# Kernel optimization log

Measured on AMD Instinct MI355X. Metric: run time of the kernel, lower is better.

## Reference

```python
import jax, jax.numpy as jnp
import numpy as np

NUM_EMBEDDINGS = 1024
EMBEDDING_DIM = 64
COMMITMENT_COST = 0.25


def setup_inputs() -> dict:
    key = jax.random.key(0)
    k1, k2 = jax.random.split(key)
    inputs = jax.random.normal(k1, (32, 4096, EMBEDDING_DIM), dtype=jnp.float32)
    embeddings = jax.random.normal(k2, (NUM_EMBEDDINGS, EMBEDDING_DIM), dtype=jnp.float32)
    return {"inputs": inputs, "embeddings": embeddings}


def _l2_normalize(x, axis=-1, eps=1e-12):
    # matches F.normalize(p=2): x / max(||x||, eps)
    n = jnp.sqrt(jnp.sum(x * x, axis=axis, keepdims=True))
    return x / jnp.maximum(n, eps)


def reference(inputs, embeddings):
    input_shape = inputs.shape
    flat = inputs.reshape(-1, EMBEDDING_DIM)            # [N, D]
    flat_n = _l2_normalize(flat, axis=1)                # [N, D]
    emb_n = _l2_normalize(embeddings, axis=1)           # [K, D]

    # squared euclidean distances between normalized vectors: [N, K]
    d = (jnp.sum(flat_n * flat_n, axis=1, keepdims=True)
         + jnp.sum(emb_n * emb_n, axis=1)
         - 2.0 * flat_n @ emb_n.T)
    idx = jnp.argmin(d, axis=1)                         # [N] int

    quantized = embeddings[idx]                         # [N, D] gather

    e_latent_loss = jnp.mean((jax.lax.stop_gradient(quantized) - flat) ** 2)
    # straight-through estimator
    quantized_ste = flat + jax.lax.stop_gradient(quantized - flat)
    q_latent_loss = jnp.mean((quantized_ste - jax.lax.stop_gradient(flat)) ** 2)
    vq_loss = q_latent_loss + COMMITMENT_COST * e_latent_loss

    quantized_out = quantized_ste.reshape(input_shape)

    counts = jnp.bincount(idx, length=NUM_EMBEDDINGS).astype(jnp.float32)
    avg_probs = counts / idx.shape[0]
    perplexity = jnp.exp(-jnp.sum(avg_probs * jnp.log(avg_probs + 1e-10)))
    codebook_usage = jnp.sum(avg_probs > 0).astype(jnp.float32) / NUM_EMBEDDINGS

    return quantized_out, idx, vq_loss, perplexity, codebook_usage
```

## Files before the change

kernel.cpp:

```cpp
#include <hip/hip_runtime.h>
#include <hip/hip_bf16.h>

#define NQ       131072
#define KC       1024
#define DIM      64
#define MARGIN_A 7.5e-5f
#define RGRID    2048

typedef __attribute__((ext_vector_type(8))) short  s8bf;
typedef __attribute__((ext_vector_type(4))) float  f32x4;

union BF8 { s8bf v; unsigned short u[8]; };

__device__ __forceinline__ unsigned short f2bf_u(float f) {
    union { __hip_bfloat16 h; unsigned short u; } cv;
    cv.h = __float2bfloat16(f);
    return cv.u;
}
__device__ __forceinline__ float bfu2f(unsigned short u) {
    union { __hip_bfloat16 h; unsigned short u; } cv;
    cv.u = u;
    return __bfloat162float(cv.h);
}

__global__ __launch_bounds__(256) void k_prep(const float* __restrict__ emb,
                                              unsigned short* __restrict__ wB,
                                              double* __restrict__ eT,
                                              double* __restrict__ wB2D,
                                              int* __restrict__ counts,
                                              int* __restrict__ nflag,
                                              float* __restrict__ lossp) {
    const int tid = threadIdx.x;
    if (blockIdx.x == 0) {
        #pragma unroll
        for (int i = 0; i < 4; ++i) counts[tid * 4 + i] = 0;
        if (tid == 0) { *nflag = 0; *lossp = 0.f; }
    }
    int c = blockIdx.x * 256 + tid;
    if (c >= KC) return;
    float e[DIM];
    const float4* ep = reinterpret_cast<const float4*>(emb + (size_t)c * DIM);
    #pragma unroll
    for (int i = 0; i < 16; ++i) {
        float4 t = ep[i];
        e[4*i+0] = t.x; e[4*i+1] = t.y; e[4*i+2] = t.z; e[4*i+3] = t.w;
    }
    float s = 0.f;
    #pragma unroll
    for (int i = 0; i < DIM; ++i) s += e[i] * e[i];
    float inv = 1.0f / fmaxf(sqrtf(s), 1e-12f);
    const int t = c >> 4, col = c & 15;
    #pragma unroll
    for (int k = 0; k < DIM; ++k) {
        float h = e[k] * inv;
        unsigned short hi = f2bf_u(h);
        unsigned short lo = f2bf_u(h - bfu2f(hi));
        int s_ = k >> 5, g = (k >> 3) & 3, j = k & 7;
        int ln = col + 16 * g;
        wB[((t*4 + s_*2 + 0) * 64 + ln) * 8 + j] = hi;
        wB[((t*4 + s_*2 + 1) * 64 + ln) * 8 + j] = lo;
    }
    double sd = 0.0;
    #pragma unroll
    for (int i = 0; i < DIM; ++i) sd += (double)e[i] * (double)e[i];
    double dnd = fmax(sqrt(sd), 1e-12);
    double b2 = 0.0;
    #pragma unroll
    for (int i = 0; i < DIM; ++i) {
        double eh = (double)e[i] / dnd;
        eT[(size_t)i * KC + c] = eh;
        b2 += eh * eh;
    }
    wB2D[c] = b2;
}

__global__ __launch_bounds__(256) void k_assign(const float* __restrict__ inp,
                                                const unsigned short* __restrict__ wB,
                                                float* __restrict__ idx_out,
                                                int* __restrict__ flag_list,
                                                int* __restrict__ nflag) {
    const int tid  = threadIdx.x;
    const int lane = tid & 63, wv = tid >> 6;
    const int col  = lane & 15, g  = lane >> 4;
    const int qbase = blockIdx.x * 128 + wv * 32;

    BF8 ah[2][2], al[2][2];
    #pragma unroll
    for (int s = 0; s < 2; ++s) {
        const float4* q4 = reinterpret_cast<const float4*>(inp + (size_t)(qbase + 16*s + col) * DIM);
        float4 xa = q4[2*g], xb = q4[2*g + 1], ya = q4[8 + 2*g], yb = q4[9 + 2*g];
        float x[16] = { xa.x, xa.y, xa.z, xa.w, xb.x, xb.y, xb.z, xb.w,
                        ya.x, ya.y, ya.z, ya.w, yb.x, yb.y, yb.z, yb.w };
        float sq = 0.f;
        #pragma unroll
        for (int i = 0; i < 16; ++i) sq += x[i] * x[i];
        sq += __shfl_xor(sq, 16);
        sq += __shfl_xor(sq, 32);
        float ninv = -1.0f / fmaxf(sqrtf(sq), 1e-12f);
        #pragma unroll
        for (int i = 0; i < 8; ++i) {
            float h0 = x[i] * ninv, h1 = x[8 + i] * ninv;
            unsigned short hi0 = f2bf_u(h0);
            unsigned short hi1 = f2bf_u(h1);
            ah[s][0].u[i] = hi0;  al[s][0].u[i] = f2bf_u(h0 - bfu2f(hi0));
            ah[s][1].u[i] = hi1;  al[s][1].u[i] = f2bf_u(h1 - bfu2f(hi1));
        }
    }

    int best[2][4], best2[2][4];
    #pragma unroll
    for (int s = 0; s < 2; ++s)
        #pragma unroll
        for (int r = 0; r < 4; ++r) { best[s][r] = 0x7FFFFFFF; best2[s][r] = 0x7FFFFFFF; }

    const s8bf* wBs = reinterpret_cast<const s8bf*>(wB);
    s8bf nb0 = wBs[0*64 + lane];
    s8bf nb1 = wBs[1*64 + lane];
    s8bf nb2 = wBs[2*64 + lane];
    s8bf nb3 = wBs[3*64 + lane];

    for (int gt = 0; gt < 64; ++gt) {
        s8bf bh0 = nb0, bl0 = nb1, bh1 = nb2, bl1 = nb3;
        if (gt < 63) {
            const s8bf* p = wBs + (gt + 1) * 4 * 64 + lane;
            nb0 = p[0]; nb1 = p[64]; nb2 = p[128]; nb3 = p[192];
        }
        #pragma unroll
        for (int s = 0; s < 2; ++s) {
            f32x4 acc = {1.5f, 1.5f, 1.5f, 1.5f};
            acc = __builtin_amdgcn_mfma_f32_16x16x32_bf16(ah[s][0].v, bh0, acc, 0, 0, 0);
            acc = __builtin_amdgcn_mfma_f32_16x16x32_bf16(ah[s][1].v, bh1, acc, 0, 0, 0);
            acc = __builtin_amdgcn_mfma_f32_16x16x32_bf16(ah[s][0].v, bl0, acc, 0, 0, 0);
            acc = __builtin_amdgcn_mfma_f32_16x16x32_bf16(ah[s][1].v, bl1, acc, 0, 0, 0);
            acc = __builtin_amdgcn_mfma_f32_16x16x32_bf16(al[s][0].v, bh0, acc, 0, 0, 0);
            acc = __builtin_amdgcn_mfma_f32_16x16x32_bf16(al[s][1].v, bh1, acc, 0, 0, 0);
            #pragma unroll
            for (int r = 0; r < 4; ++r) {
                int p = (__float_as_int(acc[r]) & 0xFFFFFFC0) | gt;
                int bo = best[s][r];
                int b2n;
                asm("v_med3_i32 %0, %1, %2, %3"
                    : "=v"(b2n) : "v"(bo), "v"(best2[s][r]), "v"(p));
                best2[s][r] = b2n;
                best[s][r]  = min(bo, p);
            }
        }
    }

    int colb[2][4];
    #pragma unroll
    for (int s = 0; s < 2; ++s)
        #pragma unroll
        for (int r = 0; r < 4; ++r) colb[s][r] = col;

    #pragma unroll
    for (int s = 0; s < 2; ++s) {
        #pragma unroll
        for (int off = 1; off < 16; off <<= 1) {
            #pragma unroll
            for (int r = 0; r < 4; ++r) {
                int ob  = __shfl_xor(best[s][r],  off);
                int ob2 = __shfl_xor(best2[s][r], off);
                int oc  = __shfl_xor(colb[s][r],  off);
                int bo  = best[s][r];
                colb[s][r]  = (ob < bo) ? oc : colb[s][r];
                best[s][r]  = min(bo, ob);
                best2[s][r] = min(min(best2[s][r], ob2), max(bo, ob));
            }
        }
        #pragma unroll
        for (int r = 0; r < 4; ++r) {
            if (col == r) {
                int   q  = qbase + 16*s + 4*g + r;
                int   pk = best[s][r];
                float a1 = __int_as_float(pk & 0xFFFFFFC0);
                float a2 = __int_as_float(best2[s][r] & 0xFFFFFFC0);
                int code = ((pk & 63) << 4) | colb[s][r];
                idx_out[q] = (float)code;
                if (a2 - a1 < MARGIN_A) {
                    int slot = atomicAdd(nflag, 1);
                    flag_list[slot] = q;
                }
            }
        }
    }
}

__global__ __launch_bounds__(256) void k_rescue(const float* __restrict__ inp,
                                                const double* __restrict__ eT,
                                                const double* __restrict__ wB2D,
                                                const int* __restrict__ flag_list,
                                                const int* __restrict__ nflag,
                                                float* __restrict__ idx_out) {
    __shared__ double xh[DIM];
    __shared__ double Ash;
    __shared__ double sdw[4];
    __shared__ int    siw[4];
    const int tid = threadIdx.x;
    const int lane = tid & 63, wv = tid >> 6;
    const int n = *nflag;

    for (int j = blockIdx.x; j < n; j += gridDim.x) {
        const int q = flag_list[j];
        if (tid < 64) {
            double xv = (double)inp[(size_t)q * DIM + tid];
            double s = xv * xv;
            #pragma unroll
            for (int off = 32; off; off >>= 1) s += __shfl_xor(s, off);
            double dn = fmax(sqrt(s), 1e-12);
            double h  = xv / dn;
            xh[tid] = h;
            double a = h * h;
            #pragma unroll
            for (int off = 32; off; off >>= 1) a += __shfl_xor(a, off);
            if (tid == 0) Ash = a;
        }
        __syncthreads();
        const double A = Ash;

        double dot0 = 0.0, dot1 = 0.0, dot2 = 0.0, dot3 = 0.0;
        #pragma unroll 8
        for (int i = 0; i < DIM; ++i) {
            double xi = xh[i];
            const double* row = eT + (size_t)i * KC + tid;
            dot0 += xi * row[0];
            dot1 += xi * row[256];
            dot2 += xi * row[512];
            dot3 += xi * row[768];
        }
        double bd = 1e300; int bi = 1 << 30;
        double d0 = (A + wB2D[tid      ]) - 2.0 * dot0;
        double d1 = (A + wB2D[tid + 256]) - 2.0 * dot1;
        double d2 = (A + wB2D[tid + 512]) - 2.0 * dot2;
        double d3 = (A + wB2D[tid + 768]) - 2.0 * dot3;
        if (d0 < bd) { bd = d0; bi = tid;       }
        if (d1 < bd) { bd = d1; bi = tid + 256; }
        if (d2 < bd) { bd = d2; bi = tid + 512; }
        if (d3 < bd) { bd = d3; bi = tid + 768; }
        #pragma unroll
        for (int off = 1; off < 64; off <<= 1) {
            double od = __shfl_xor(bd, off);
            int    oi = __shfl_xor(bi, off);
            if (od < bd || (od == bd && oi < bi)) { bd = od; bi = oi; }
        }
        if (lane == 0) { sdw[wv] = bd; siw[wv] = bi; }
        __syncthreads();
        if (tid == 0) {
            double B = sdw[0]; int I = siw[0];
            #pragma unroll
            for (int i = 1; i < 4; ++i)
                if (sdw[i] < B || (sdw[i] == B && siw[i] < I)) { B = sdw[i]; I = siw[i]; }
            idx_out[q] = (float)I;
        }
        __syncthreads();
    }
}

__global__ __launch_bounds__(256) void k_gather_loss(const float* __restrict__ inp,
                                                     const float* __restrict__ emb,
                                                     const float* __restrict__ idx_out,
                                                     float* __restrict__ qout,
                                                     float* __restrict__ loss,
                                                     int* __restrict__ counts) {
    __shared__ int h[KC];
    const int tid = threadIdx.x;
    for (int i = tid; i < KC; i += 256) h[i] = 0;
    __syncthreads();

    const int gid = blockIdx.x * 256 + tid;
    float lsum = 0.f;
    for (int e4 = gid; e4 < NQ * 16; e4 += 524288) {
        int   qi = e4 >> 4;
        int   d4 = e4 & 15;
        int   k  = ((int)idx_out[qi]) & (KC - 1);
        float4 qv = reinterpret_cast<const float4*>(emb + (size_t)k * DIM)[d4];
        float4 fv = reinterpret_cast<const float4*>(inp)[e4];
        float ux = qv.x - fv.x, uy = qv.y - fv.y, uz = qv.z - fv.z, uw = qv.w - fv.w;
        lsum += ux*ux + uy*uy + uz*uz + uw*uw;
        reinterpret_cast<float4*>(qout)[e4] = qv;
        if (d4 == 0) atomicAdd(&h[k], 1);
    }
    __syncthreads();
    for (int i = tid; i < KC; i += 256) {
        int v = h[i];
        if (v) atomicAdd(&counts[i], v);
    }
    #pragma unroll
    for (int off = 32; off; off >>= 1) lsum += __shfl_xor(lsum, off);
    __shared__ float wsum[4];
    int wid = tid >> 6, lane = tid & 63;
    if (lane == 0) wsum[wid] = lsum;
    __syncthreads();
    if (tid == 0)
        atomicAdd(loss, (wsum[0] + wsum[1]) + (wsum[2] + wsum[3]));
}

__global__ __launch_bounds__(1024) void k_stats2(const int* __restrict__ counts,
                                                 float* __restrict__ out3) {
    int t = threadIdx.x;
    int c = counts[t];
    float p    = (float)c * (1.0f / (float)NQ);
    float ent  = p * logf(p + 1e-10f);
    float used = (c > 0) ? 1.0f : 0.0f;
    #pragma unroll
    for (int off = 32; off; off >>= 1) {
        ent  += __shfl_xor(ent, off);
        used += __shfl_xor(used, off);
    }
    __shared__ float se[16], su[16];
    int w = t >> 6, l = t & 63;
    if (l == 0) { se[w] = ent; su[w] = used; }
    __syncthreads();
    if (t == 0) {
        float E = 0.f, U = 0.f;
        #pragma unroll
        for (int i = 0; i < 16; ++i) { E += se[i]; U += su[i]; }
        float L = out3[0];
        out3[0] = L * 1.25f / 8388608.0f;
        out3[1] = expf(-E);
        out3[2] = U * (1.0f / 1024.0f);
    }
}

extern "C" void kernel_launch(void* const* d_in, const int* in_sizes, int n_in,
                              void* d_out, int out_size, void* d_ws, size_t ws_size,
                              hipStream_t stream) {
    const float* inp = (const float*)d_in[0];
    const float* emb = (const float*)d_in[1];

    float*  qout      = (float*)d_out;
    int*    flag_list = (int*)d_out;
    double* eT        = (double*)((float*)d_out + 1048576);
    float*  idx_out   = (float*)d_out + 8388608;
    float*  out3      = (float*)d_out + 8519680;

    int*            counts = (int*)d_ws;
    unsigned short* wB     = (unsigned short*)((char*)d_ws + 4096);
    double*         wB2D   = (double*)((char*)d_ws + 266240);
    int*            nflag  = (int*)((char*)d_ws + 274432);

    hipLaunchKernelGGL(k_prep,        dim3(4),     dim3(256),  0, stream,
                       emb, wB, eT, wB2D, counts, nflag, out3);
    hipLaunchKernelGGL(k_assign,      dim3(1024),  dim3(256),  0, stream,
                       inp, wB, idx_out, flag_list, nflag);
    hipLaunchKernelGGL(k_rescue,      dim3(RGRID), dim3(256),  0, stream,
                       inp, eT, wB2D, flag_list, nflag, idx_out);
    hipLaunchKernelGGL(k_gather_loss, dim3(2048),  dim3(256),  0, stream,
                       inp, emb, idx_out, qout, out3, counts);
    hipLaunchKernelGGL(k_stats2,      dim3(1),     dim3(1024), 0, stream, counts, out3);
}
```

Before: 118.8 us.

## Switch assignment to 32x32x16 MFMA tiles and parallelize codebook prep per element

The assignment kernel now uses 32x32x16 bf16 MFMA instructions with a 32-code tile per iteration (32 iterations instead of 64). The codebook pre-pack layout and the A-operand register layout change to match. This halves the per-tile argmin bookkeeping per code and raises MFMA efficiency. The prep kernel also moves from one thread per code with serial loops to one 64-lane wave per code using shuffle reductions, which removes the long serial prologue. The larger accumulator raises register pressure, and the final cross-lane reduction now takes 5 shuffle steps over 16 values.

```diff
diff --git a/kernel.cpp b/kernel.cpp
--- a/kernel.cpp
+++ b/kernel.cpp
@@ -7,8 +7,8 @@
 #define MARGIN_A 7.5e-5f
 #define RGRID    2048
 
-typedef __attribute__((ext_vector_type(8))) short  s8bf;
-typedef __attribute__((ext_vector_type(4))) float  f32x4;
+typedef __attribute__((ext_vector_type(8)))  short s8bf;
+typedef __attribute__((ext_vector_type(16))) float f32x16;
 
 union BF8 { s8bf v; unsigned short u[8]; };
 
@@ -23,55 +23,43 @@
     return __bfloat162float(cv.h);
 }
 
-__global__ __launch_bounds__(256) void k_prep(const float* __restrict__ emb,
-                                              unsigned short* __restrict__ wB,
-                                              double* __restrict__ eT,
-                                              double* __restrict__ wB2D,
-                                              int* __restrict__ counts,
-                                              int* __restrict__ nflag,
-                                              float* __restrict__ lossp) {
-    const int tid = threadIdx.x;
-    if (blockIdx.x == 0) {
-        #pragma unroll
-        for (int i = 0; i < 4; ++i) counts[tid * 4 + i] = 0;
-        if (tid == 0) { *nflag = 0; *lossp = 0.f; }
-    }
-    int c = blockIdx.x * 256 + tid;
-    if (c >= KC) return;
-    float e[DIM];
-    const float4* ep = reinterpret_cast<const float4*>(emb + (size_t)c * DIM);
-    #pragma unroll
-    for (int i = 0; i < 16; ++i) {
-        float4 t = ep[i];
-        e[4*i+0] = t.x; e[4*i+1] = t.y; e[4*i+2] = t.z; e[4*i+3] = t.w;
-    }
-    float s = 0.f;
-    #pragma unroll
-    for (int i = 0; i < DIM; ++i) s += e[i] * e[i];
-    float inv = 1.0f / fmaxf(sqrtf(s), 1e-12f);
-    const int t = c >> 4, col = c & 15;
-    #pragma unroll
-    for (int k = 0; k < DIM; ++k) {
-        float h = e[k] * inv;
-        unsigned short hi = f2bf_u(h);
-        unsigned short lo = f2bf_u(h - bfu2f(hi));
-        int s_ = k >> 5, g = (k >> 3) & 3, j = k & 7;
-        int ln = col + 16 * g;
-        wB[((t*4 + s_*2 + 0) * 64 + ln) * 8 + j] = hi;
-        wB[((t*4 + s_*2 + 1) * 64 + ln) * 8 + j] = lo;
-    }
-    double sd = 0.0;
-    #pragma unroll
-    for (int i = 0; i < DIM; ++i) sd += (double)e[i] * (double)e[i];
+__global__ __launch_bounds__(64) void k_prep(const float* __restrict__ emb,
+                                             unsigned short* __restrict__ wB,
+                                             double* __restrict__ eT,
+                                             double* __restrict__ wB2D,
+                                             int* __restrict__ counts,
+                                             int* __restrict__ nflag,
+                                             float* __restrict__ lossp) {
+    const int c = blockIdx.x;
+    const int i = threadIdx.x;
+    if (i == 0) counts[c] = 0;
+    if (c == 0 && i == 0) { *nflag = 0; *lossp = 0.f; }
+
+    float e = emb[(size_t)c * DIM + i];
+    float sq = e * e;
+    #pragma unroll
+    for (int off = 1; off < 64; off <<= 1) sq += __shfl_xor(sq, off);
+    float inv = 1.0f / fmaxf(sqrtf(sq), 1e-12f);
+    float h = e * inv;
+    unsigned short hi = f2bf_u(h);
+    unsigned short lo = f2bf_u(h - bfu2f(hi));
+    const int t = c >> 5, col = c & 31;
+    const int ks = i >> 4, hh = (i >> 3) & 1, j = i & 7;
+    const int ln = col + 32 * hh;
+    wB[(((t*8 + ks*2 + 0) * 64) + ln) * 8 + j] = hi;
+    wB[(((t*8 + ks*2 + 1) * 64) + ln) * 8 + j] = lo;
+
+    double ed = (double)e;
+    double sd = ed * ed;
+    #pragma unroll
+    for (int off = 1; off < 64; off <<= 1) sd += __shfl_xor(sd, off);
     double dnd = fmax(sqrt(sd), 1e-12);
-    double b2 = 0.0;
-    #pragma unroll
-    for (int i = 0; i < DIM; ++i) {
-        double eh = (double)e[i] / dnd;
-        eT[(size_t)i * KC + c] = eh;
-        b2 += eh * eh;
-    }
-    wB2D[c] = b2;
+    double eh  = ed / dnd;
+    eT[(size_t)i * KC + c] = eh;
+    double b2 = eh * eh;
+    #pragma unroll
+    for (int off = 1; off < 64; off <<= 1) b2 += __shfl_xor(b2, off);
+    if (i == 0) wB2D[c] = b2;
 }
 
 __global__ __launch_bounds__(256) void k_assign(const float* __restrict__ inp,
@@ -81,106 +69,110 @@
                                                 int* __restrict__ nflag) {
     const int tid  = threadIdx.x;
     const int lane = tid & 63, wv = tid >> 6;
-    const int col  = lane & 15, g  = lane >> 4;
+    const int m  = lane & 31;
+    const int hh = lane >> 5;
     const int qbase = blockIdx.x * 128 + wv * 32;
 
-    BF8 ah[2][2], al[2][2];
-    #pragma unroll
-    for (int s = 0; s < 2; ++s) {
-        const float4* q4 = reinterpret_cast<const float4*>(inp + (size_t)(qbase + 16*s + col) * DIM);
-        float4 xa = q4[2*g], xb = q4[2*g + 1], ya = q4[8 + 2*g], yb = q4[9 + 2*g];
-        float x[16] = { xa.x, xa.y, xa.z, xa.w, xb.x, xb.y, xb.z, xb.w,
-                        ya.x, ya.y, ya.z, ya.w, yb.x, yb.y, yb.z, yb.w };
+    BF8 ah[4], al[4];
+    {
+        const float4* qp = reinterpret_cast<const float4*>(inp + (size_t)(qbase + m) * DIM);
+        float x[32];
+        #pragma unroll
+        for (int ks = 0; ks < 4; ++ks) {
+            float4 a = qp[4*ks + 2*hh];
+            float4 b = qp[4*ks + 2*hh + 1];
+            x[8*ks+0]=a.x; x[8*ks+1]=a.y; x[8*ks+2]=a.z; x[8*ks+3]=a.w;
+            x[8*ks+4]=b.x; x[8*ks+5]=b.y; x[8*ks+6]=b.z; x[8*ks+7]=b.w;
+        }
         float sq = 0.f;
         #pragma unroll
-        for (int i = 0; i < 16; ++i) sq += x[i] * x[i];
-        sq += __shfl_xor(sq, 16);
+        for (int i = 0; i < 32; ++i) sq += x[i] * x[i];
         sq += __shfl_xor(sq, 32);
         float ninv = -1.0f / fmaxf(sqrtf(sq), 1e-12f);
         #pragma unroll
-        for (int i = 0; i < 8; ++i) {
-            float h0 = x[i] * ninv, h1 = x[8 + i] * ninv;
-            unsigned short hi0 = f2bf_u(h0);
-            unsigned short hi1 = f2bf_u(h1);
-            ah[s][0].u[i] = hi0;  al[s][0].u[i] = f2bf_u(h0 - bfu2f(hi0));
-            ah[s][1].u[i] = hi1;  al[s][1].u[i] = f2bf_u(h1 - bfu2f(hi1));
-        }
-    }
-
-    int best[2][4], best2[2][4];
-    #pragma unroll
-    for (int s = 0; s < 2; ++s)
-        #pragma unroll
-        for (int r = 0; r < 4; ++r) { best[s][r] = 0x7FFFFFFF; best2[s][r] = 0x7FFFFFFF; }
+        for (int ks = 0; ks < 4; ++ks)
+            #pragma unroll
+            for (int j = 0; j < 8; ++j) {
+                float h = x[8*ks+j] * ninv;
+                unsigned short hi = f2bf_u(h);
+                ah[ks].u[j] = hi;
+                al[ks].u[j] = f2bf_u(h - bfu2f(hi));
+            }
+    }
+
+    int best[16], best2[16];
+    #pragma unroll
+    for (int r = 0; r < 16; ++r) { best[r] = 0x7FFFFFFF; best2[r] = 0x7FFFFFFF; }
 
     const s8bf* wBs = reinterpret_cast<const s8bf*>(wB);
-    s8bf nb0 = wBs[0*64 + lane];
-    s8bf nb1 = wBs[1*64 + lane];
-    s8bf nb2 = wBs[2*64 + lane];
-    s8bf nb3 = wBs[3*64 + lane];
-
-    for (int gt = 0; gt < 64; ++gt) {
+    s8bf nb0 = wBs[0*64 + lane], nb1 = wBs[1*64 + lane];
+    s8bf nb2 = wBs[2*64 + lane], nb3 = wBs[3*64 + lane];
+    s8bf nb4 = wBs[4*64 + lane], nb5 = wBs[5*64 + lane];
+    s8bf nb6 = wBs[6*64 + lane], nb7 = wBs[7*64 + lane];
+
+    for (int gt = 0; gt < 32; ++gt) {
         s8bf bh0 = nb0, bl0 = nb1, bh1 = nb2, bl1 = nb3;
-        if (gt < 63) {
-            const s8bf* p = wBs + (gt + 1) * 4 * 64 + lane;
-            nb0 = p[0]; nb1 = p[64]; nb2 = p[128]; nb3 = p[192];
-        }
-        #pragma unroll
-        for (int s = 0; s < 2; ++s) {
-            f32x4 acc = {1.5f, 1.5f, 1.5f, 1.5f};
-            acc = __builtin_amdgcn_mfma_f32_16x16x32_bf16(ah[s][0].v, bh0, acc, 0, 0, 0);
-            acc = __builtin_amdgcn_mfma_f32_16x16x32_bf16(ah[s][1].v, bh1, acc, 0, 0, 0);
-            acc = __builtin_amdgcn_mfma_f32_16x16x32_bf16(ah[s][0].v, bl0, acc, 0, 0, 0);
-            acc = __builtin_amdgcn_mfma_f32_16x16x32_bf16(ah[s][1].v, bl1, acc, 0, 0, 0);
-            acc = __builtin_amdgcn_mfma_f32_16x16x32_bf16(al[s][0].v, bh0, acc, 0, 0, 0);
-            acc = __builtin_amdgcn_mfma_f32_16x16x32_bf16(al[s][1].v, bh1, acc, 0, 0, 0);
-            #pragma unroll
-            for (int r = 0; r < 4; ++r) {
-                int p = (__float_as_int(acc[r]) & 0xFFFFFFC0) | gt;
-                int bo = best[s][r];
-                int b2n;
-                asm("v_med3_i32 %0, %1, %2, %3"
-                    : "=v"(b2n) : "v"(bo), "v"(best2[s][r]), "v"(p));
-                best2[s][r] = b2n;
-                best[s][r]  = min(bo, p);
-            }
-        }
-    }
-
-    int colb[2][4];
-    #pragma unroll
-    for (int s = 0; s < 2; ++s)
-        #pragma unroll
-        for (int r = 0; r < 4; ++r) colb[s][r] = col;
-
-    #pragma unroll
-    for (int s = 0; s < 2; ++s) {
-        #pragma unroll
-        for (int off = 1; off < 16; off <<= 1) {
-            #pragma unroll
-            for (int r = 0; r < 4; ++r) {
-                int ob  = __shfl_xor(best[s][r],  off);
-                int ob2 = __shfl_xor(best2[s][r], off);
-                int oc  = __shfl_xor(colb[s][r],  off);
-                int bo  = best[s][r];
-                colb[s][r]  = (ob < bo) ? oc : colb[s][r];
-                best[s][r]  = min(bo, ob);
-                best2[s][r] = min(min(best2[s][r], ob2), max(bo, ob));
-            }
-        }
-        #pragma unroll
-        for (int r = 0; r < 4; ++r) {
-            if (col == r) {
-                int   q  = qbase + 16*s + 4*g + r;
-                int   pk = best[s][r];
-                float a1 = __int_as_float(pk & 0xFFFFFFC0);
-                float a2 = __int_as_float(best2[s][r] & 0xFFFFFFC0);
-                int code = ((pk & 63) << 4) | colb[s][r];
-                idx_out[q] = (float)code;
-                if (a2 - a1 < MARGIN_A) {
-                    int slot = atomicAdd(nflag, 1);
-                    flag_list[slot] = q;
-                }
+        s8bf bh2 = nb4, bl2 = nb5, bh3 = nb6, bl3 = nb7;
+        if (gt < 31) {
+            const s8bf* p = wBs + (size_t)(gt + 1) * 8 * 64 + lane;
+            nb0 = p[0];   nb1 = p[64];  nb2 = p[128]; nb3 = p[192];
+            nb4 = p[256]; nb5 = p[320]; nb6 = p[384]; nb7 = p[448];
+        }
+        f32x16 acc = {1.5f,1.5f,1.5f,1.5f,1.5f,1.5f,1.5f,1.5f,
+                      1.5f,1.5f,1.5f,1.5f,1.5f,1.5f,1.5f,1.5f};
+        acc = __builtin_amdgcn_mfma_f32_32x32x16_bf16(ah[0].v, bh0, acc, 0, 0, 0);
+        acc = __builtin_amdgcn_mfma_f32_32x32x16_bf16(ah[1].v, bh1, acc, 0, 0, 0);
+        acc = __builtin_amdgcn_mfma_f32_32x32x16_bf16(ah[2].v, bh2, acc, 0, 0, 0);
+        acc = __builtin_amdgcn_mfma_f32_32x32x16_bf16(ah[3].v, bh3, acc, 0, 0, 0);
+        acc = __builtin_amdgcn_mfma_f32_32x32x16_bf16(ah[0].v, bl0, acc, 0, 0, 0);
+        acc = __builtin_amdgcn_mfma_f32_32x32x16_bf16(al[0].v, bh0, acc, 0, 0, 0);
+        acc = __builtin_amdgcn_mfma_f32_32x32x16_bf16(ah[1].v, bl1, acc, 0, 0, 0);
+        acc = __builtin_amdgcn_mfma_f32_32x32x16_bf16(al[1].v, bh1, acc, 0, 0, 0);
+        acc = __builtin_amdgcn_mfma_f32_32x32x16_bf16(ah[2].v, bl2, acc, 0, 0, 0);
+        acc = __builtin_amdgcn_mfma_f32_32x32x16_bf16(al[2].v, bh2, acc, 0, 0, 0);
+        acc = __builtin_amdgcn_mfma_f32_32x32x16_bf16(ah[3].v, bl3, acc, 0, 0, 0);
+        acc = __builtin_amdgcn_mfma_f32_32x32x16_bf16(al[3].v, bh3, acc, 0, 0, 0);
+        #pragma unroll
+        for (int r = 0; r < 16; ++r) {
+            int p = (__float_as_int(acc[r]) & 0xFFFFFFC0) | gt;
+            int bo = best[r];
+            int b2n;
+            asm("v_med3_i32 %0, %1, %2, %3"
+                : "=v"(b2n) : "v"(bo), "v"(best2[r]), "v"(p));
+            best2[r] = b2n;
+            best[r]  = min(bo, p);
+        }
+    }
+
+    int colb[16];
+    #pragma unroll
+    for (int r = 0; r < 16; ++r) colb[r] = m;
+
+    #pragma unroll
+    for (int off = 1; off < 32; off <<= 1) {
+        #pragma unroll
+        for (int r = 0; r < 16; ++r) {
+            int ob  = __shfl_xor(best[r],  off);
+            int ob2 = __shfl_xor(best2[r], off);
+            int oc  = __shfl_xor(colb[r],  off);
+            int bo  = best[r];
+            colb[r]  = (ob < bo) ? oc : colb[r];
+            best[r]  = min(bo, ob);
+            best2[r] = min(min(best2[r], ob2), max(bo, ob));
+        }
+    }
+    #pragma unroll
+    for (int r = 0; r < 16; ++r) {
+        if (m == r) {
+            int   q  = qbase + (r & 3) + 8 * (r >> 2) + 4 * hh;
+            int   pk = best[r];
+            float a1 = __int_as_float(pk & 0xFFFFFFC0);
+            float a2 = __int_as_float(best2[r] & 0xFFFFFFC0);
+            int code = ((pk & 63) << 5) | colb[r];
+            idx_out[q] = (float)code;
+            if (a2 - a1 < MARGIN_A) {
+                int slot = atomicAdd(nflag, 1);
+                flag_list[slot] = q;
             }
         }
     }
@@ -339,13 +331,13 @@
     double*         wB2D   = (double*)((char*)d_ws + 266240);
     int*            nflag  = (int*)((char*)d_ws + 274432);
 
-    hipLaunchKernelGGL(k_prep,        dim3(4),     dim3(256),  0, stream,
+    hipLaunchKernelGGL(k_prep,        dim3(1024), dim3(64),   0, stream,
                        emb, wB, eT, wB2D, counts, nflag, out3);
-    hipLaunchKernelGGL(k_assign,      dim3(1024),  dim3(256),  0, stream,
+    hipLaunchKernelGGL(k_assign,      dim3(1024), dim3(256),  0, stream,
                        inp, wB, idx_out, flag_list, nflag);
-    hipLaunchKernelGGL(k_rescue,      dim3(RGRID), dim3(256),  0, stream,
+    hipLaunchKernelGGL(k_rescue,      dim3(RGRID), dim3(256), 0, stream,
                        inp, eT, wB2D, flag_list, nflag, idx_out);
-    hipLaunchKernelGGL(k_gather_loss, dim3(2048),  dim3(256),  0, stream,
+    hipLaunchKernelGGL(k_gather_loss, dim3(2048), dim3(256),  0, stream,
                        inp, emb, idx_out, qout, out3, counts);
-    hipLaunchKernelGGL(k_stats2,      dim3(1),     dim3(1024), 0, stream, counts, out3);
-}
+    hipLaunchKernelGGL(k_stats2,      dim3(1),    dim3(1024), 0, stream, counts, out3);
+}
```

Measured after the change: 129.5 us. 1.09x slower.
